# Kernel tuning notes

Measured on AMD Instinct MI355X. Metric: run time of the kernel, lower is better.

The kernel has to match this reference:

```python
import jax, jax.numpy as jnp
import numpy as np

K, D, P, C = 96, 256, 40, 8  # trials, embed dim, phoneme bins, gate hidden

def setup_inputs() -> dict:
    key = jax.random.key(0)
    ks = jax.random.split(key, 5)
    return {
        "enroll": jax.random.normal(ks[0], (K, D, P), jnp.float32),
        "test": jax.random.normal(ks[1], (K, D, P), jnp.float32),
        "fc1_w": jax.random.normal(ks[2], (C, 1), jnp.float32) * 0.5,
        "fc1_b": jax.random.normal(ks[3], (C,), jnp.float32) * 0.1,
        "fc2_w": jax.random.normal(ks[4], (1, C), jnp.float32) * 0.5,
    }

def _l2norm(x, axis):
    # torch F.normalize(p=2): x / max(||x||, eps)
    n = jnp.sqrt(jnp.sum(x * x, axis=axis, keepdims=True))
    return x / jnp.maximum(n, 1e-12)

def _gate(x, fc1_w, fc1_b, fc2_w):
    # tiny 1->C->1 MLP: fc2(tanh(fc1(x))), applied elementwise on x
    h = jnp.tanh(x[..., None] * fc1_w[:, 0] + fc1_b)   # [..., C]
    return jnp.einsum('...c,c->...', h, fc2_w[0])

def reference(enroll, test, fc1_w, fc1_b, fc2_w):
    e = _l2norm(enroll, axis=1)                        # [K, D, P]
    t = _l2norm(test, axis=1)                          # [K, D, P]
    # pho_matrix[k,l,i,j] = <e[k,:,i], t[l,:,j]>
    pho = jnp.einsum('kdi,ldj->klij', e, t)            # [K, K, P, P]
    cnt1 = jnp.sum(pho != 0, axis=-1).astype(pho.dtype) + 1e-6
    pho = _gate(pho, fc1_w, fc1_b, fc2_w) * pho        # gated elementwise
    pho = jnp.sum(pho, axis=-1) / cnt1                 # [K, K, P]
    cnt2 = jnp.sum(pho != 0, axis=-1).astype(pho.dtype) + 1e-6
    pho = _gate(pho, fc1_w, fc1_b, fc2_w) * pho        # [K, K, P]
    return jnp.sum(pho, axis=-1) / cnt2                # [K, K]
```

## Files before the change

### kernel.cpp

```cpp
#include <hip/hip_runtime.h>
#include <math.h>

#define KTR 96
#define DIM 256
#define PB  40
#define CH  8
#define MDIM 3840
#define KK  512
#define BM 160
#define BN 64
#define BK 32
#define LDA 40
#define NTAB 2113
#define TPAD 2120

typedef _Float16 v8h __attribute__((ext_vector_type(8)));
typedef float    v4f __attribute__((ext_vector_type(4)));

__device__ __forceinline__ float gate_ref(float x, const float* w, const float* b, const float* v) {
    float g = 0.f;
    #pragma unroll
    for (int c = 0; c < CH; ++c) g = fmaf(v[c], tanhf(fmaf(w[c], x, b[c])), g);
    return g;
}

__global__ __launch_bounds__(256) void k_norm(const float* __restrict__ enroll,
                                              const float* __restrict__ test,
                                              const float* __restrict__ fc1_w,
                                              const float* __restrict__ fc1_b,
                                              const float* __restrict__ fc2_w,
                                              _Float16* __restrict__ XT,
                                              _Float16* __restrict__ XE,
                                              float2* __restrict__ gtabG) {
    int b = blockIdx.x, tid = threadIdx.x;

    if (b >= 2 * KTR) {
        int i = (b - 2 * KTR) * 256 + tid;
        if (i < NTAB) {
            float w[CH], bb[CH], vv[CH];
            #pragma unroll
            for (int c = 0; c < CH; ++c) { w[c] = fc1_w[c]; bb[c] = fc1_b[c]; vv[c] = fc2_w[c]; }
            float g0 = gate_ref((float)(i - 1056) * 0.0009765625f, w, bb, vv);
            float g1 = gate_ref((float)(i - 1055) * 0.0009765625f, w, bb, vv);
            gtabG[i] = make_float2(g0, g1 - g0);
        }
        return;
    }

    bool isE = (b < KTR);
    int k = isE ? b : b - KTR;
    const float* src = (isE ? enroll : test) + (size_t)k * DIM * PB;

    __shared__ float S[DIM * 41];
    __shared__ float part[6 * PB];
    __shared__ float rn[PB];

    for (int i = tid; i < DIM * PB / 4; i += 256) {
        float4 v = ((const float4*)src)[i];
        int d = i / 10, c = i - d * 10;
        float* p = &S[d * 41 + c * 4];
        p[0] = v.x; p[1] = v.y; p[2] = v.z; p[3] = v.w;
    }
    __syncthreads();
    if (tid < 240) {
        int g = tid / PB, p = tid - (tid / PB) * PB;
        float acc = 0.f;
        for (int d = g; d < DIM; d += 6) {
            float x = S[d * 41 + p];
            acc = fmaf(x, x, acc);
        }
        part[g * PB + p] = acc;
    }
    __syncthreads();
    if (tid < PB) {
        float s = 0.f;
        #pragma unroll
        for (int g = 0; g < 6; ++g) s += part[g * PB + tid];
        rn[tid] = 1.0f / fmaxf(sqrtf(s), 1e-12f);
    }
    __syncthreads();

    int d = tid;
    for (int p = 0; p < PB; ++p) {
        float v = S[d * 41 + p] * rn[p];
        _Float16 h  = (_Float16)v;
        _Float16 lo = (_Float16)((v - (float)h) * 4096.0f);
        size_t m = (size_t)(k * PB + p);
        if (isE) { XE[m * KK + d] = lo; XE[m * KK + 256 + d] = h;  }
        else     { XT[m * KK + d] = h;  XT[m * KK + 256 + d] = lo; }
    }
}

__global__ __launch_bounds__(256, 2) void k_gemm(const _Float16* __restrict__ XT,
                                                 const _Float16* __restrict__ XE,
                                                 const float2* __restrict__ gtabG,
                                                 float* __restrict__ pho2) {
    __shared__ __align__(16) _Float16 LA[BM * LDA];
    __shared__ __align__(16) _Float16 LB[BN * LDA];
    __shared__ float2 gtab[TPAD];

    int tid  = threadIdx.x;
    int lane = tid & 63;
    int wv   = tid >> 6;

    for (int i = tid; i < NTAB; i += 256) gtab[i] = gtabG[i];

    int id = blockIdx.y * 60 + blockIdx.x;
    int wg = (id & 7) * 180 + (id >> 3);
    int m0 = (wg / 60) * BM;
    int n0 = (wg % 60) * BN;
    int wm = (wv & 1) * 80;
    int wn = (wv >> 1) * 32;
    int r15 = lane & 15;
    int q4  = lane >> 4;

    v4f acc[5][2];
    #pragma unroll
    for (int mt = 0; mt < 5; ++mt)
        #pragma unroll
        for (int nt = 0; nt < 2; ++nt)
            acc[mt][nt] = (v4f)0.f;

    int aoff[5], boff[2];
    #pragma unroll
    for (int mt = 0; mt < 5; ++mt) aoff[mt] = (wm + mt * 16 + r15) * LDA + q4 * 8;
    #pragma unroll
    for (int nt = 0; nt < 2; ++nt) boff[nt] = (wn + nt * 16 + r15) * LDA + q4 * 8;

    int arow = tid >> 2, aqc = tid & 3;
    const uint4* gT = (const uint4*)(XT + (size_t)(m0 + arow) * KK);
    const uint4* gE = (const uint4*)(XE + (size_t)(n0 + arow) * KK);
    uint4* lA = (uint4*)LA + (arow * 5 + aqc);
    uint4* lB = (uint4*)LB + (arow * 5 + aqc);

    uint4 va0, va1, va2, vb0;
    #define LOADS(IT) {                                                     \
        int ka = ((IT) < 16) ? (IT) * BK : ((IT) - 16) * BK;                \
        int kb = ((IT) < 16) ? (IT) * BK : 256 + ((IT) - 16) * BK;          \
        int ia = (ka >> 3) + aqc, ib = (kb >> 3) + aqc;                     \
        va0 = gT[ia]; va1 = gT[ia + 64 * 64];                               \
        if (tid < 128) va2 = gT[ia + 128 * 64];                             \
        vb0 = gE[ib]; }

    LOADS(0);
    for (int it = 0; it < 24; ++it) {
        __syncthreads();
        lA[0]   = va0;
        lA[320] = va1;
        if (tid < 128) lA[640] = va2;
        lB[0]   = vb0;
        __syncthreads();

        if (it < 23) LOADS(it + 1);

        if (it == 16) {
            #pragma unroll
            for (int mt = 0; mt < 5; ++mt)
                #pragma unroll
                for (int nt = 0; nt < 2; ++nt)
                    acc[mt][nt] *= 0.000244140625f;
        }

        v8h af[5], bf[2];
        #pragma unroll
        for (int mt = 0; mt < 5; ++mt) af[mt] = *(const v8h*)(LA + aoff[mt]);
        #pragma unroll
        for (int nt = 0; nt < 2; ++nt) bf[nt] = *(const v8h*)(LB + boff[nt]);
        #pragma unroll
        for (int mt = 0; mt < 5; ++mt)
            #pragma unroll
            for (int nt = 0; nt < 2; ++nt)
                acc[mt][nt] = __builtin_amdgcn_mfma_f32_16x16x32_f16(af[mt], bf[nt], acc[mt][nt], 0, 0, 0);
    }
    #undef LOADS

    const float inv40 = 1.0f / (40.0f + 1e-6f);
    int lg = (m0 + wm) / PB;
    #pragma unroll
    for (int nt = 0; nt < 2; ++nt) {
        float s0 = 0.f, s1 = 0.f, t2 = 0.f;
        #pragma unroll
        for (int mt = 0; mt < 5; ++mt) {
            #pragma unroll
            for (int r = 0; r < 4; ++r) {
                float x = acc[mt][nt][r];
                float u = fmaf(x, 1024.0f, 1056.0f);
                int i = (int)u;
                i = min(max(i, 0), NTAB - 2);
                float f = u - (float)i;
                float2 t = gtab[i];
                float g = fmaf(f, t.y, t.x);
                float xg = g * x;
                if (mt < 2)       s0 += xg;
                else if (mt == 2) t2 += xg;
                else              s1 += xg;
            }
        }
        bool lo = (q4 < 2);
        s0 += lo ? t2 : 0.f;
        s1 += lo ? 0.f : t2;
        s0 += __shfl_xor(s0, 16); s0 += __shfl_xor(s0, 32);
        s1 += __shfl_xor(s1, 16); s1 += __shfl_xor(s1, 32);
        if (q4 == 0) {
            int n = n0 + wn + nt * 16 + r15;
            int kk = n / PB, ii = n - kk * PB;
            pho2[((size_t)kk * KTR + lg)     * PB + ii] = s0 * inv40;
            pho2[((size_t)kk * KTR + lg + 1) * PB + ii] = s1 * inv40;
        }
    }
}

__global__ __launch_bounds__(256) void k_final(const float* __restrict__ pho2,
                                               const float* __restrict__ fc1_w,
                                               const float* __restrict__ fc1_b,
                                               const float* __restrict__ fc2_w,
                                               float* __restrict__ out) {
    int wv = threadIdx.x >> 6;
    int lane = threadIdx.x & 63;
    int pair = blockIdx.x * 4 + wv;

    float w[CH], bb[CH], vv[CH];
    #pragma unroll
    for (int c = 0; c < CH; ++c) { w[c] = fc1_w[c]; bb[c] = fc1_b[c]; vv[c] = fc2_w[c]; }

    float x = (lane < PB) ? pho2[(size_t)pair * PB + lane] : 0.f;
    float s = gate_ref(x, w, bb, vv) * x;

    #pragma unroll
    for (int off = 32; off; off >>= 1) s += __shfl_xor(s, off);
    if (lane == 0) out[pair] = s / (40.0f + 1e-6f);
}

extern "C" void kernel_launch(void* const* d_in, const int* in_sizes, int n_in,
                              void* d_out, int out_size, void* d_ws, size_t ws_size,
                              hipStream_t stream) {
    const float* enroll = (const float*)d_in[0];
    const float* test   = (const float*)d_in[1];
    const float* fc1_w  = (const float*)d_in[2];
    const float* fc1_b  = (const float*)d_in[3];
    const float* fc2_w  = (const float*)d_in[4];
    float* out = (float*)d_out;

    _Float16* XT = (_Float16*)d_ws;
    _Float16* XE = XT + (size_t)MDIM * KK;
    float* pho2  = (float*)(XE + (size_t)MDIM * KK);
    float2* gtabG = (float2*)(pho2 + (size_t)KTR * KTR * PB);

    k_norm<<<2 * KTR + 9, 256, 0, stream>>>(enroll, test, fc1_w, fc1_b, fc2_w, XT, XE, gtabG);
    dim3 g2(MDIM / BN, MDIM / BM);
    k_gemm<<<g2, 256, 0, stream>>>(XT, XE, gtabG, pho2);
    k_final<<<KTR * KTR / 4, 256, 0, stream>>>(pho2, fc1_w, fc1_b, fc2_w, out);
}
```

Measured before the change: 117.0 us.

## Load MFMA fragments directly from global memory, bypassing LDS staging

```diff
diff --git a/kernel.cpp b/kernel.cpp
--- a/kernel.cpp
+++ b/kernel.cpp
@@ -10,7 +10,6 @@
 #define BM 160
 #define BN 64
 #define BK 32
-#define LDA 40
 #define NTAB 2113
 #define TPAD 2120
 
@@ -95,15 +94,18 @@
                                                  const _Float16* __restrict__ XE,
                                                  const float2* __restrict__ gtabG,
                                                  float* __restrict__ pho2) {
-    __shared__ __align__(16) _Float16 LA[BM * LDA];
-    __shared__ __align__(16) _Float16 LB[BN * LDA];
-    __shared__ float2 gtab[TPAD];
+    __shared__ float gval[TPAD];
+    __shared__ float gslope[TPAD];
 
     int tid  = threadIdx.x;
     int lane = tid & 63;
     int wv   = tid >> 6;
 
-    for (int i = tid; i < NTAB; i += 256) gtab[i] = gtabG[i];
+    for (int i = tid; i < NTAB; i += 256) {
+        float2 t = gtabG[i];
+        gval[i] = t.x; gslope[i] = t.y;
+    }
+    __syncthreads();
 
     int id = blockIdx.y * 60 + blockIdx.x;
     int wg = (id & 7) * 180 + (id >> 3);
@@ -121,38 +123,30 @@
         for (int nt = 0; nt < 2; ++nt)
             acc[mt][nt] = (v4f)0.f;
 
-    int aoff[5], boff[2];
-    #pragma unroll
-    for (int mt = 0; mt < 5; ++mt) aoff[mt] = (wm + mt * 16 + r15) * LDA + q4 * 8;
-    #pragma unroll
-    for (int nt = 0; nt < 2; ++nt) boff[nt] = (wn + nt * 16 + r15) * LDA + q4 * 8;
-
-    int arow = tid >> 2, aqc = tid & 3;
-    const uint4* gT = (const uint4*)(XT + (size_t)(m0 + arow) * KK);
-    const uint4* gE = (const uint4*)(XE + (size_t)(n0 + arow) * KK);
-    uint4* lA = (uint4*)LA + (arow * 5 + aqc);
-    uint4* lB = (uint4*)LB + (arow * 5 + aqc);
-
-    uint4 va0, va1, va2, vb0;
-    #define LOADS(IT) {                                                     \
+    const _Float16* pa[5];
+    const _Float16* pb[2];
+    #pragma unroll
+    for (int mt = 0; mt < 5; ++mt) pa[mt] = XT + (size_t)(m0 + wm + mt * 16 + r15) * KK + q4 * 8;
+    #pragma unroll
+    for (int nt = 0; nt < 2; ++nt) pb[nt] = XE + (size_t)(n0 + wn + nt * 16 + r15) * KK + q4 * 8;
+
+    v8h Aa[5], Ab[2], Ba[5], Bb[2];
+
+    #define GLD(Sa, Sb, IT) {                                               \
         int ka = ((IT) < 16) ? (IT) * BK : ((IT) - 16) * BK;                \
         int kb = ((IT) < 16) ? (IT) * BK : 256 + ((IT) - 16) * BK;          \
-        int ia = (ka >> 3) + aqc, ib = (kb >> 3) + aqc;                     \
-        va0 = gT[ia]; va1 = gT[ia + 64 * 64];                               \
-        if (tid < 128) va2 = gT[ia + 128 * 64];                             \
-        vb0 = gE[ib]; }
-
-    LOADS(0);
-    for (int it = 0; it < 24; ++it) {
-        __syncthreads();
-        lA[0]   = va0;
-        lA[320] = va1;
-        if (tid < 128) lA[640] = va2;
-        lB[0]   = vb0;
-        __syncthreads();
-
-        if (it < 23) LOADS(it + 1);
-
+        _Pragma("unroll") for (int mt = 0; mt < 5; ++mt) Sa[mt] = *(const v8h*)(pa[mt] + ka); \
+        _Pragma("unroll") for (int nt = 0; nt < 2; ++nt) Sb[nt] = *(const v8h*)(pb[nt] + kb); }
+
+    #define MFMAS(Sa, Sb) {                                                 \
+        _Pragma("unroll") for (int mt = 0; mt < 5; ++mt)                    \
+        _Pragma("unroll") for (int nt = 0; nt < 2; ++nt)                    \
+            acc[mt][nt] = __builtin_amdgcn_mfma_f32_16x16x32_f16(Sa[mt], Sb[nt], acc[mt][nt], 0, 0, 0); }
+
+    GLD(Aa, Ab, 0);
+    #pragma unroll
+    for (int it = 0; it < 24; it += 2) {
+        GLD(Ba, Bb, it + 1);
         if (it == 16) {
             #pragma unroll
             for (int mt = 0; mt < 5; ++mt)
@@ -160,19 +154,12 @@
                 for (int nt = 0; nt < 2; ++nt)
                     acc[mt][nt] *= 0.000244140625f;
         }
-
-        v8h af[5], bf[2];
-        #pragma unroll
-        for (int mt = 0; mt < 5; ++mt) af[mt] = *(const v8h*)(LA + aoff[mt]);
-        #pragma unroll
-        for (int nt = 0; nt < 2; ++nt) bf[nt] = *(const v8h*)(LB + boff[nt]);
-        #pragma unroll
-        for (int mt = 0; mt < 5; ++mt)
-            #pragma unroll
-            for (int nt = 0; nt < 2; ++nt)
-                acc[mt][nt] = __builtin_amdgcn_mfma_f32_16x16x32_f16(af[mt], bf[nt], acc[mt][nt], 0, 0, 0);
-    }
-    #undef LOADS
+        MFMAS(Aa, Ab);
+        if (it + 2 < 24) GLD(Aa, Ab, it + 2);
+        MFMAS(Ba, Bb);
+    }
+    #undef GLD
+    #undef MFMAS
 
     const float inv40 = 1.0f / (40.0f + 1e-6f);
     int lg = (m0 + wm) / PB;
@@ -188,8 +175,7 @@
                 int i = (int)u;
                 i = min(max(i, 0), NTAB - 2);
                 float f = u - (float)i;
-                float2 t = gtab[i];
-                float g = fmaf(f, t.y, t.x);
+                float g = fmaf(f, gslope[i], gval[i]);
                 float xg = g * x;
                 if (mt < 2)       s0 += xg;
                 else if (mt == 2) t2 += xg;
```

After: 174.4 us. 1.49x slower.
